# Optimization experiments

Hardware: AMD Instinct MI355X
Metric: run time of the kernel (lower is better)

Reference implementation:

```python
import jax, jax.numpy as jnp
import numpy as np

NUM_TREES = 150
ARITY = 4
DEPTH = 4
NUM_LEVELS = DEPTH + 1  # leaves (level 0) ... root (level DEPTH)
VOCAB = 10000
SUBTOK = 8
EMB_DIM = 256
HID = 256
NUM_CLASSES = 2


def _build_forest():
    # perfect ARITY-ary tree, level-order indexing; edges point child -> parent
    n = (ARITY ** (DEPTH + 1) - 1) // (ARITY - 1)  # 341
    src = np.arange(1, n)
    dst = (src - 1) // ARITY
    depth_of = np.zeros(n, dtype=np.int64)
    for j in range(1, n):
        depth_of[j] = depth_of[(j - 1) // ARITY] + 1
    level_of = DEPTH - depth_of  # leaves = 0, processed first (topo order)
    offs = np.arange(NUM_TREES) * n
    edge_src = (src[None, :] + offs[:, None]).ravel().astype(np.int32)
    edge_dst = (dst[None, :] + offs[:, None]).ravel().astype(np.int32)
    node_level = np.tile(level_of, NUM_TREES).astype(np.int32)
    graph_id = np.repeat(np.arange(NUM_TREES), n).astype(np.int32)
    leaf_mask = (node_level == 0).astype(np.int32)
    return edge_src, edge_dst, node_level, graph_id, leaf_mask, NUM_TREES * n


def setup_inputs() -> dict:
    key = jax.random.key(0)
    ks = jax.random.split(key, 16)
    es, ed, lvl, gid, lm, N = _build_forest()
    s_e = 1.0 / np.sqrt(EMB_DIM)
    s_h = 1.0 / np.sqrt(HID)
    s_f = 1.0 / np.sqrt(2 * HID)
    return {
        "node_feat1": jax.random.randint(ks[0], (N, SUBTOK), 0, VOCAB, dtype=jnp.int32),
        "node_feat2": jax.random.randint(ks[1], (N, SUBTOK), 0, VOCAB, dtype=jnp.int32),
        "emb1": jax.random.normal(ks[2], (VOCAB, EMB_DIM), jnp.float32) * 0.02,
        "emb2": jax.random.normal(ks[3], (VOCAB, EMB_DIM), jnp.float32) * 0.02,
        "W_iou1": jax.random.normal(ks[4], (EMB_DIM, 3 * HID), jnp.float32) * s_e,
        "W_iou2": jax.random.normal(ks[5], (EMB_DIM, 3 * HID), jnp.float32) * s_e,
        "U_iou1": jax.random.normal(ks[6], (HID, 3 * HID), jnp.float32) * s_h,
        "U_iou2": jax.random.normal(ks[7], (HID, 3 * HID), jnp.float32) * s_h,
        "Uf_W1": jax.random.normal(ks[8], (HID, HID), jnp.float32) * s_h,
        "Uf_b1": jnp.zeros((HID,), jnp.float32),
        "Uf_W2": jax.random.normal(ks[9], (HID, HID), jnp.float32) * s_h,
        "Uf_b2": jnp.zeros((HID,), jnp.float32),
        "b_iou1": jnp.zeros((3 * HID,), jnp.float32),
        "b_iou2": jnp.zeros((3 * HID,), jnp.float32),
        "Wf": jax.random.normal(ks[10], (2 * HID, NUM_CLASSES), jnp.float32) * s_f,
        "bf": jnp.zeros((NUM_CLASSES,), jnp.float32),
        "edge_src": jnp.asarray(es),
        "edge_dst": jnp.asarray(ed),
        "node_level": jnp.asarray(lvl),
        "graph_id": jnp.asarray(gid),
        "leaf_mask": jnp.asarray(lm),
    }


def _tree_lstm(iou0, U_iou, Uf_W, Uf_b, b_iou, edge_src, edge_dst, node_level):
    # ChildSum TreeLSTM, propagated level-by-level (leaves -> root)
    N = iou0.shape[0]
    h = jnp.zeros((N, HID), iou0.dtype)
    c = jnp.zeros((N, HID), iou0.dtype)
    for lvl in range(NUM_LEVELS):
        emask = (node_level[edge_dst] == lvl).astype(h.dtype)[:, None]  # [E,1]
        hs = h[edge_src] * emask  # children h (already computed at lower levels)
        f = jax.nn.sigmoid(hs @ Uf_W + Uf_b)  # per-edge forget gate
        h_tild = jax.ops.segment_sum(hs, edge_dst, num_segments=N)
        c_sum = jax.ops.segment_sum(f * c[edge_src] * emask, edge_dst, num_segments=N)
        has_child = jax.ops.segment_sum(emask, edge_dst, num_segments=N) > 0  # [N,1]
        # DGL semantics: reduce overwrites iou for internal nodes; leaves keep W_iou(x)*mask
        iou = jnp.where(has_child, h_tild @ U_iou, iou0) + b_iou
        i, o, u = jnp.split(iou, 3, axis=1)
        c_new = jax.nn.sigmoid(i) * jnp.tanh(u) + c_sum
        h_new = jax.nn.sigmoid(o) * jnp.tanh(c_new)
        at = (node_level == lvl)[:, None]
        h = jnp.where(at, h_new, h)
        c = jnp.where(at, c_new, c)
    return h


def _branch(node_feat, emb, W_iou, U_iou, Uf_W, Uf_b, b_iou,
            leaf_mask, edge_src, edge_dst, node_level, graph_id):
    embeds = emb[node_feat].mean(axis=1)  # subtoken mean pooling -> [N, EMB_DIM]
    iou0 = (embeds @ W_iou) * leaf_mask.astype(embeds.dtype)[:, None]
    h = _tree_lstm(iou0, U_iou, Uf_W, Uf_b, b_iou, edge_src, edge_dst, node_level)
    s = jax.ops.segment_sum(h, graph_id, num_segments=NUM_TREES)
    cnt = jax.ops.segment_sum(jnp.ones((h.shape[0],), h.dtype), graph_id, num_segments=NUM_TREES)
    return jax.nn.relu(s / cnt[:, None])  # mean graph readout + relu


def reference(node_feat1, node_feat2, emb1, emb2, W_iou1, W_iou2, U_iou1, U_iou2,
              Uf_W1, Uf_b1, Uf_W2, Uf_b2, b_iou1, b_iou2, Wf, bf,
              edge_src, edge_dst, node_level, graph_id, leaf_mask):
    m1 = _branch(node_feat1, emb1, W_iou1, U_iou1, Uf_W1, Uf_b1, b_iou1,
                 leaf_mask, edge_src, edge_dst, node_level, graph_id)
    m2 = _branch(node_feat2, emb2, W_iou2, U_iou2, Uf_W2, Uf_b2, b_iou2,
                 leaf_mask, edge_src, edge_dst, node_level, graph_id)
    logits = jax.nn.leaky_relu(jnp.concatenate([m1, m2], axis=1) @ Wf + bf, 0.01)
    return jax.nn.softmax(logits, axis=-1)
```

## Files before the change

kernel.cpp:

```cpp
#include <hip/hip_runtime.h>

#define NT 150
#define NPT 341
#define LEAF0 85
#define NL (NT*256)
#define NN (NT*NPT)
#define VOCAB 10000

typedef __attribute__((ext_vector_type(8))) short short8;
typedef __attribute__((ext_vector_type(4))) float floatx4;

__device__ __forceinline__ float sigf(float x){
  return __builtin_amdgcn_rcpf(1.0f + __expf(-x));
}
__device__ __forceinline__ float tanh_fast(float x){
  float e = __expf(2.0f*x);
  return 1.0f - 2.0f*__builtin_amdgcn_rcpf(e + 1.0f);
}
__device__ __forceinline__ float bf2f(ushort u){ union{unsigned i; float f;} v; v.i = ((unsigned)u)<<16; return v.f; }
__device__ __forceinline__ ushort f2bf(float x){ union{float f; unsigned i;} v; v.f = x; return (ushort)((v.i + 0x7fff + ((v.i>>16)&1))>>16); }

__global__ __launch_bounds__(256) void prep_k(
    const float* __restrict__ e1, const float* __restrict__ e2,
    ushort* __restrict__ E1, ushort* __restrict__ E2,
    const float* __restrict__ W1, const float* __restrict__ U1, const float* __restrict__ F1,
    const float* __restrict__ W2, const float* __restrict__ U2, const float* __restrict__ F2,
    ushort* Wt1, ushort* Ut1, ushort* Ft1, ushort* Wt2, ushort* Ut2, ushort* Ft2){
  __shared__ float T[32][33];
  int bid = blockIdx.x;
  if (bid < 5000){
    const float* s = (bid >= 2500) ? e2 : e1;
    ushort* d = (bid >= 2500) ? E2 : E1;
    size_t i = ((size_t)(bid % 2500)*256 + threadIdx.x)*4;
    float4 v = *(const float4*)&s[i];
    d[i+0]=f2bf(v.x); d[i+1]=f2bf(v.y); d[i+2]=f2bf(v.z); d[i+3]=f2bf(v.w);
    return;
  }
  int w = bid - 5000;
  int z = w / 192, rem = w % 192;
  int bx = rem % 24, by = rem / 24;
  const float* src; ushort* dst; int N;
  switch (z){
    case 0: src=W1; dst=Wt1; N=768; break;
    case 1: src=U1; dst=Ut1; N=768; break;
    case 2: src=F1; dst=Ft1; N=256; break;
    case 3: src=W2; dst=Wt2; N=768; break;
    case 4: src=U2; dst=Ut2; N=768; break;
    default: src=F2; dst=Ft2; N=256; break;
  }
  int n0 = bx*32; if (n0 >= N) return;
  int k0 = by*32;
  int nl = threadIdx.x & 31, kb = threadIdx.x >> 5;
  #pragma unroll
  for (int i=0;i<4;i++){ int kk = kb*4+i; T[kk][nl] = src[(size_t)(k0+kk)*N + n0 + nl]; }
  __syncthreads();
  #pragma unroll
  for (int i=0;i<4;i++){ int nn = kb*4+i; dst[(size_t)(n0+nn)*256 + k0 + nl] = f2bf(T[nl][nn]); }
}

__global__ __launch_bounds__(512) void leaf_gemm(
    const int* __restrict__ f1, const int* __restrict__ f2,
    const ushort* __restrict__ E1, const ushort* __restrict__ E2,
    const ushort* __restrict__ Wt1, const float* __restrict__ b1,
    const ushort* __restrict__ Wt2, const float* __restrict__ b2,
    ushort* __restrict__ h1, ushort* __restrict__ c1,
    ushort* __restrict__ h2, ushort* __restrict__ c2){
  __shared__ __attribute__((aligned(16))) ushort As[8][32*40];
  int br = blockIdx.y;
  const int* feat = br ? f2 : f1;
  const ushort* E = br ? E2 : E1;
  const ushort* Wt = br ? Wt2 : Wt1;
  const float* biou = br ? b2 : b1;
  ushort* h = br ? h2 : h1;
  ushort* c = br ? c2 : c1;
  int tid = threadIdx.x;
  int lane = tid & 63, wav = tid >> 6, quad = lane >> 4, l15 = lane & 15;
  int rowbase = blockIdx.x*32;

  {
    int row = tid >> 4, seg = tid & 15;
    int leaf = rowbase + row;
    int tree = leaf >> 8;
    size_t node = (size_t)tree*NPT + LEAF0 + (leaf & 255);
    const int* f = feat + node*8;
    int4 fA = *(const int4*)f;
    int4 fB = *(const int4*)(f+4);
    int idx[8] = {fA.x, fA.y, fA.z, fA.w, fB.x, fB.y, fB.z, fB.w};
    float s[16];
    #pragma unroll
    for (int q=0;q<16;q++) s[q]=0.f;
    #pragma unroll
    for (int half=0; half<2; half++){
      short8 va[4], vb[4];
      #pragma unroll
      for (int j=0;j<4;j++){
        const ushort* rowp = E + (size_t)idx[half*4+j]*256 + seg*16;
        va[j] = *(const short8*)rowp;
        vb[j] = *(const short8*)(rowp+8);
      }
      #pragma unroll
      for (int j=0;j<4;j++){
        #pragma unroll
        for (int q=0;q<8;q++){ s[q]+=bf2f((ushort)va[j][q]); s[8+q]+=bf2f((ushort)vb[j][q]); }
      }
    }
    short8 o1, o2;
    #pragma unroll
    for (int q=0;q<8;q++){ o1[q]=(short)f2bf(s[q]*0.125f); o2[q]=(short)f2bf(s[8+q]*0.125f); }
    int cch = seg >> 1, off = (seg & 1)*16;
    *(short8*)&As[cch][row*40 + off]     = o1;
    *(short8*)&As[cch][row*40 + off + 8] = o2;
  }
  __syncthreads();

  floatx4 acc[3][2][2];
  #pragma unroll
  for (int g=0;g<3;g++)
    #pragma unroll
    for (int cg=0;cg<2;cg++)
      #pragma unroll
      for (int r=0;r<2;r++) acc[g][cg][r] = (floatx4){0.f,0.f,0.f,0.f};

  const ushort* bp[3][2];
  #pragma unroll
  for (int g=0;g<3;g++)
    #pragma unroll
    for (int cg=0;cg<2;cg++)
      bp[g][cg] = Wt + (size_t)(g*256 + cg*128 + wav*16 + l15)*256 + quad*8;

  #pragma unroll
  for (int cch=0; cch<8; cch++){
    short8 B[3][2];
    #pragma unroll
    for (int g=0;g<3;g++)
      #pragma unroll
      for (int cg=0;cg<2;cg++) B[g][cg] = *(const short8*)(bp[g][cg] + cch*32);
    #pragma unroll
    for (int r=0;r<2;r++){
      short8 a = *(const short8*)&As[cch][(16*r + l15)*40 + quad*8];
      #pragma unroll
      for (int g=0;g<3;g++)
        #pragma unroll
        for (int cg=0;cg<2;cg++)
          acc[g][cg][r] = __builtin_amdgcn_mfma_f32_16x16x32_bf16(a, B[g][cg], acc[g][cg][r], 0,0,0);
    }
  }
  #pragma unroll
  for (int cg=0;cg<2;cg++){
    int hc = cg*128 + wav*16 + l15;
    float bi = biou[hc], bo = biou[256+hc], bu = biou[512+hc];
    #pragma unroll
    for (int r=0;r<2;r++){
      #pragma unroll
      for (int reg=0;reg<4;reg++){
        int leaf = rowbase + 16*r + quad*4 + reg;
        int tree = leaf >> 8;
        size_t node = (size_t)tree*NPT + LEAF0 + (leaf & 255);
        float iv = acc[0][cg][r][reg] + bi;
        float ov = acc[1][cg][r][reg] + bo;
        float uv = acc[2][cg][r][reg] + bu;
        float cc = sigf(iv)*tanh_fast(uv);
        float hh = sigf(ov)*tanh_fast(cc);
        h[node*256 + hc] = f2bf(hh);
        c[node*256 + hc] = f2bf(cc);
      }
    }
  }
}

__global__ __launch_bounds__(512) void level_k(
    const ushort* __restrict__ Ut1, const ushort* __restrict__ Ft1,
    const float* __restrict__ Ufb1, const float* __restrict__ bi1,
    const ushort* __restrict__ Ut2, const ushort* __restrict__ Ft2,
    const float* __restrict__ Ufb2, const float* __restrict__ bi2,
    ushort* __restrict__ h1, ushort* __restrict__ c1,
    ushort* __restrict__ h2, ushort* __restrict__ c2,
    int M, int shift, int base){
  __shared__ __attribute__((aligned(16))) ushort Ch[8][64*40];
  int br = blockIdx.z;
  const ushort* Ut = br ? Ut2 : Ut1;
  const ushort* Ft = br ? Ft2 : Ft1;
  const float* Ufb = br ? Ufb2 : Ufb1;
  const float* biou = br ? bi2 : bi1;
  ushort* h = br ? h2 : h1;
  ushort* c = br ? c2 : c1;
  int tid = threadIdx.x;
  int lane = tid & 63, wav = tid >> 6, quad = lane >> 4, l15 = lane & 15;
  int m0 = blockIdx.x*16;
  int mask = (1<<shift)-1;

  {
    int cl = tid >> 3, s8 = tid & 7;
    int sm = m0 + (cl >> 2); if (sm > M-1) sm = M-1;
    int stree = sm >> shift, sloc = base + (sm & mask);
    const ushort* sgp = h + ((size_t)stree*NPT + 4*sloc + 1 + (cl & 3))*256 + s8*32;
    short8 v0 = *(const short8*)(sgp);
    short8 v1 = *(const short8*)(sgp+8);
    short8 v2 = *(const short8*)(sgp+16);
    short8 v3 = *(const short8*)(sgp+24);
    *(short8*)&Ch[s8][cl*40 + 0]  = v0;
    *(short8*)&Ch[s8][cl*40 + 8]  = v1;
    *(short8*)&Ch[s8][cl*40 + 16] = v2;
    *(short8*)&Ch[s8][cl*40 + 24] = v3;
  }
  __syncthreads();

  int col = blockIdx.y*128 + wav*16 + l15;
  const ushort* bfp = Ft + (size_t)col*256 + quad*8;
  const ushort* bp0 = Ut + (size_t)(0*256 + col)*256 + quad*8;
  const ushort* bp1 = Ut + (size_t)(256 + col)*256 + quad*8;
  const ushort* bp2 = Ut + (size_t)(512 + col)*256 + quad*8;

  floatx4 af[4], ai[4], ao[4], au[4];
  #pragma unroll
  for (int r=0;r<4;r++){
    af[r] = (floatx4){0.f,0.f,0.f,0.f}; ai[r] = (floatx4){0.f,0.f,0.f,0.f};
    ao[r] = (floatx4){0.f,0.f,0.f,0.f}; au[r] = (floatx4){0.f,0.f,0.f,0.f};
  }

  #pragma unroll
  for (int cc=0; cc<8; cc++){
    short8 Bf = *(const short8*)(bfp + cc*32);
    short8 Bi = *(const short8*)(bp0 + cc*32);
    short8 Bo = *(const short8*)(bp1 + cc*32);
    short8 Bu = *(const short8*)(bp2 + cc*32);
    #pragma unroll
    for (int r=0;r<4;r++){
      short8 a = *(const short8*)&Ch[cc][(16*r + l15)*40 + quad*8];
      af[r] = __builtin_amdgcn_mfma_f32_16x16x32_bf16(a, Bf, af[r], 0,0,0);
      ai[r] = __builtin_amdgcn_mfma_f32_16x16x32_bf16(a, Bi, ai[r], 0,0,0);
      ao[r] = __builtin_amdgcn_mfma_f32_16x16x32_bf16(a, Bo, ao[r], 0,0,0);
      au[r] = __builtin_amdgcn_mfma_f32_16x16x32_bf16(a, Bu, au[r], 0,0,0);
    }
  }

  float ufb = Ufb[col];
  float bI = biou[col], bO = biou[256+col], bU = biou[512+col];
  #pragma unroll
  for (int r=0;r<4;r++){
    int m = m0 + 4*r + quad;
    int mm = m < M ? m : M-1;
    int tree = mm >> shift, loc = base + (mm & mask);
    size_t ch0 = ((size_t)tree*NPT + 4*loc + 1)*256 + col;
    float cs = 0.f;
    #pragma unroll
    for (int reg=0;reg<4;reg++)
      cs += sigf(af[r][reg] + ufb) * bf2f(c[ch0 + (size_t)reg*256]);
    float iv = ai[r][0]+ai[r][1]+ai[r][2]+ai[r][3] + bI;
    float ov = ao[r][0]+ao[r][1]+ao[r][2]+ao[r][3] + bO;
    float uv = au[r][0]+au[r][1]+au[r][2]+au[r][3] + bU;
    float cn = sigf(iv)*tanh_fast(uv) + cs;
    float hn = sigf(ov)*tanh_fast(cn);
    if (m < M){
      size_t off = ((size_t)tree*NPT + loc)*256 + col;
      h[off] = f2bf(hn);
      c[off] = f2bf(cn);
    }
  }
}

__global__ __launch_bounds__(256) void readout_k(
    const ushort* __restrict__ h1, const ushort* __restrict__ h2,
    float* __restrict__ mp1, float* __restrict__ mp2){
  __shared__ float red[4][256];
  int br = blockIdx.z, part = blockIdx.y, tree = blockIdx.x;
  const ushort* h = br ? h2 : h1;
  float* mp = br ? mp2 : mp1;
  int t = threadIdx.x;
  int lane = t & 63, rg = t >> 6;
  int start = part*85;
  int cnt = (part==3) ? 86 : 85;
  const ushort* base = h + ((size_t)tree*NPT + start)*256 + lane*4;
  float s0=0.f,s1=0.f,s2=0.f,s3=0.f;
  for (int i=rg; i<cnt; i+=4){
    ushort4 v = *(const ushort4*)(base + (size_t)i*256);
    s0 += bf2f(v.x); s1 += bf2f(v.y); s2 += bf2f(v.z); s3 += bf2f(v.w);
  }
  *(float4*)&red[rg][lane*4] = make_float4(s0,s1,s2,s3);
  __syncthreads();
  float tot = red[0][t]+red[1][t]+red[2][t]+red[3][t];
  mp[((size_t)tree*4 + part)*256 + t] = tot;
}

__global__ __launch_bounds__(64) void final_k(const float* __restrict__ mp1,
    const float* __restrict__ mp2, const float* __restrict__ Wf,
    const float* __restrict__ bf, float* __restrict__ out){
  int tree = blockIdx.x; int t = threadIdx.x;
  float p0=0.f, p1=0.f;
  for (int k=t;k<512;k+=64){
    const float* mp = (k<256) ? mp1 : mp2;
    int kk = k & 255;
    size_t b0 = ((size_t)tree*4)*256 + kk;
    float s = mp[b0] + mp[b0+256] + mp[b0+512] + mp[b0+768];
    float x = fmaxf(s*(1.0f/341.0f), 0.f);
    p0 += x*Wf[k*2+0]; p1 += x*Wf[k*2+1];
  }
  #pragma unroll
  for (int off=32; off>0; off>>=1){
    p0 += __shfl_down(p0, off);
    p1 += __shfl_down(p1, off);
  }
  if (t==0){
    float l0 = p0+bf[0], l1 = p1+bf[1];
    l0 = (l0>0.f)?l0:0.01f*l0;
    l1 = (l1>0.f)?l1:0.01f*l1;
    float mx = fmaxf(l0,l1);
    float e0 = __expf(l0-mx), e1 = __expf(l1-mx);
    float inv = 1.0f/(e0+e1);
    out[tree*2+0] = e0*inv; out[tree*2+1] = e1*inv;
  }
}

extern "C" void kernel_launch(void* const* d_in, const int* in_sizes, int n_in,
                              void* d_out, int out_size, void* d_ws, size_t ws_size,
                              hipStream_t stream) {
  const int*   feat1 = (const int*)  d_in[0];
  const int*   feat2 = (const int*)  d_in[1];
  const float* emb1  = (const float*)d_in[2];
  const float* emb2  = (const float*)d_in[3];
  const float* Wiou1 = (const float*)d_in[4];
  const float* Wiou2 = (const float*)d_in[5];
  const float* Uiou1 = (const float*)d_in[6];
  const float* Uiou2 = (const float*)d_in[7];
  const float* UfW1  = (const float*)d_in[8];
  const float* Ufb1  = (const float*)d_in[9];
  const float* UfW2  = (const float*)d_in[10];
  const float* Ufb2  = (const float*)d_in[11];
  const float* biou1 = (const float*)d_in[12];
  const float* biou2 = (const float*)d_in[13];
  const float* Wf    = (const float*)d_in[14];
  const float* bfv   = (const float*)d_in[15];
  float* out = (float*)d_out;

  char* ws = (char*)d_ws;
  ushort* h1  = (ushort*)ws;  ws += (size_t)NN*256*2;
  ushort* h2  = (ushort*)ws;  ws += (size_t)NN*256*2;
  ushort* c1  = (ushort*)ws;  ws += (size_t)NN*256*2;
  ushort* c2  = (ushort*)ws;  ws += (size_t)NN*256*2;
  ushort* E1  = (ushort*)ws;  ws += (size_t)VOCAB*256*2;
  ushort* E2  = (ushort*)ws;  ws += (size_t)VOCAB*256*2;
  ushort* Wt1 = (ushort*)ws;  ws += 768*256*2;
  ushort* Ut1 = (ushort*)ws;  ws += 768*256*2;
  ushort* Ft1 = (ushort*)ws;  ws += 256*256*2;
  ushort* Wt2 = (ushort*)ws;  ws += 768*256*2;
  ushort* Ut2 = (ushort*)ws;  ws += 768*256*2;
  ushort* Ft2 = (ushort*)ws;  ws += 256*256*2;
  float*  mp1 = (float*)ws;   ws += (size_t)NT*4*256*4;
  float*  mp2 = (float*)ws;   ws += (size_t)NT*4*256*4;

  prep_k<<<dim3(6152), 256, 0, stream>>>(emb1, emb2, E1, E2,
                                         Wiou1, Uiou1, UfW1, Wiou2, Uiou2, UfW2,
                                         Wt1, Ut1, Ft1, Wt2, Ut2, Ft2);
  leaf_gemm<<<dim3(NL/32, 2), 512, 0, stream>>>(feat1, feat2, E1, E2,
                                                Wt1, biou1, Wt2, biou2,
                                                h1, c1, h2, c2);

  const int lvlM[4]     = {9600, 2400, 600, 150};
  const int lvlShift[4] = {6, 4, 2, 0};
  const int lvlBase[4]  = {21, 5, 1, 0};
  for (int l=0;l<4;l++){
    int gx = (lvlM[l] + 15)/16;
    level_k<<<dim3(gx, 2, 2), 512, 0, stream>>>(Ut1, Ft1, Ufb1, biou1,
                                                Ut2, Ft2, Ufb2, biou2,
                                                h1, c1, h2, c2,
                                                lvlM[l], lvlShift[l], lvlBase[l]);
  }
  readout_k<<<dim3(NT, 4, 2), 256, 0, stream>>>(h1, h2, mp1, mp2);
  final_k<<<NT, 64, 0, stream>>>(mp1, mp2, Wf, bfv, out);
}
```

Before: 403.5 us.

## Fuse leaf GEMM with first tree level into one kernel

Merges the leaf embedding, W_iou GEMM and the first internal level update into a single kernel with 1024-thread blocks covering 64 leaves (16 parents). Leaf h values are kept in shared memory and c in registers, so the first level's U_iou and forget-gate GEMMs run without writing leaf state to global memory and reading it back. This drops one kernel launch and one level pass. The cost is heavier per-block register and LDS use and fewer blocks overall, which may reduce occupancy.

Measured after the change: 367.4 us. 1.1x faster.

```diff
diff --git a/kernel.cpp b/kernel.cpp
--- a/kernel.cpp
+++ b/kernel.cpp
@@ -58,30 +58,37 @@
   for (int i=0;i<4;i++){ int nn = kb*4+i; dst[(size_t)(n0+nn)*256 + k0 + nl] = f2bf(T[nl][nn]); }
 }
 
-__global__ __launch_bounds__(512) void leaf_gemm(
+__global__ __launch_bounds__(1024, 4) void leaf_lvl1_k(
     const int* __restrict__ f1, const int* __restrict__ f2,
     const ushort* __restrict__ E1, const ushort* __restrict__ E2,
-    const ushort* __restrict__ Wt1, const float* __restrict__ b1,
-    const ushort* __restrict__ Wt2, const float* __restrict__ b2,
+    const ushort* __restrict__ Wt1, const ushort* __restrict__ Ut1,
+    const ushort* __restrict__ Ft1, const float* __restrict__ b1,
+    const float* __restrict__ Ufb1,
+    const ushort* __restrict__ Wt2, const ushort* __restrict__ Ut2,
+    const ushort* __restrict__ Ft2, const float* __restrict__ b2,
+    const float* __restrict__ Ufb2,
     ushort* __restrict__ h1, ushort* __restrict__ c1,
     ushort* __restrict__ h2, ushort* __restrict__ c2){
-  __shared__ __attribute__((aligned(16))) ushort As[8][32*40];
+  __shared__ __attribute__((aligned(16))) ushort As[8][64*40];
   int br = blockIdx.y;
   const int* feat = br ? f2 : f1;
   const ushort* E = br ? E2 : E1;
   const ushort* Wt = br ? Wt2 : Wt1;
+  const ushort* Ut = br ? Ut2 : Ut1;
+  const ushort* Ft = br ? Ft2 : Ft1;
   const float* biou = br ? b2 : b1;
+  const float* Ufb = br ? Ufb2 : Ufb1;
   ushort* h = br ? h2 : h1;
   ushort* c = br ? c2 : c1;
   int tid = threadIdx.x;
   int lane = tid & 63, wav = tid >> 6, quad = lane >> 4, l15 = lane & 15;
-  int rowbase = blockIdx.x*32;
+  int rowbase = blockIdx.x*64;
+  int tree = rowbase >> 8, lbase = rowbase & 255;
+  size_t tb = (size_t)tree*NPT;
 
   {
     int row = tid >> 4, seg = tid & 15;
-    int leaf = rowbase + row;
-    int tree = leaf >> 8;
-    size_t node = (size_t)tree*NPT + LEAF0 + (leaf & 255);
+    size_t node = tb + LEAF0 + lbase + row;
     const int* f = feat + node*8;
     int4 fA = *(const int4*)f;
     int4 fB = *(const int4*)(f+4);
@@ -113,58 +120,97 @@
   }
   __syncthreads();
 
-  floatx4 acc[3][2][2];
+  floatx4 acc[3][4];
   #pragma unroll
   for (int g=0;g<3;g++)
     #pragma unroll
-    for (int cg=0;cg<2;cg++)
-      #pragma unroll
-      for (int r=0;r<2;r++) acc[g][cg][r] = (floatx4){0.f,0.f,0.f,0.f};
-
-  const ushort* bp[3][2];
-  #pragma unroll
-  for (int g=0;g<3;g++)
-    #pragma unroll
-    for (int cg=0;cg<2;cg++)
-      bp[g][cg] = Wt + (size_t)(g*256 + cg*128 + wav*16 + l15)*256 + quad*8;
+    for (int r=0;r<4;r++) acc[g][r] = (floatx4){0.f,0.f,0.f,0.f};
+
+  int hc = wav*16 + l15;
+  const ushort* bp0 = Wt + (size_t)(0*256 + hc)*256 + quad*8;
+  const ushort* bp1 = Wt + (size_t)(256 + hc)*256 + quad*8;
+  const ushort* bp2 = Wt + (size_t)(512 + hc)*256 + quad*8;
 
   #pragma unroll
   for (int cch=0; cch<8; cch++){
-    short8 B[3][2];
-    #pragma unroll
-    for (int g=0;g<3;g++)
-      #pragma unroll
-      for (int cg=0;cg<2;cg++) B[g][cg] = *(const short8*)(bp[g][cg] + cch*32);
-    #pragma unroll
-    for (int r=0;r<2;r++){
+    short8 b0 = *(const short8*)(bp0 + cch*32);
+    short8 b1 = *(const short8*)(bp1 + cch*32);
+    short8 b2 = *(const short8*)(bp2 + cch*32);
+    #pragma unroll
+    for (int r=0;r<4;r++){
       short8 a = *(const short8*)&As[cch][(16*r + l15)*40 + quad*8];
-      #pragma unroll
-      for (int g=0;g<3;g++)
-        #pragma unroll
-        for (int cg=0;cg<2;cg++)
-          acc[g][cg][r] = __builtin_amdgcn_mfma_f32_16x16x32_bf16(a, B[g][cg], acc[g][cg][r], 0,0,0);
-    }
-  }
-  #pragma unroll
-  for (int cg=0;cg<2;cg++){
-    int hc = cg*128 + wav*16 + l15;
-    float bi = biou[hc], bo = biou[256+hc], bu = biou[512+hc];
-    #pragma unroll
-    for (int r=0;r<2;r++){
-      #pragma unroll
-      for (int reg=0;reg<4;reg++){
-        int leaf = rowbase + 16*r + quad*4 + reg;
-        int tree = leaf >> 8;
-        size_t node = (size_t)tree*NPT + LEAF0 + (leaf & 255);
-        float iv = acc[0][cg][r][reg] + bi;
-        float ov = acc[1][cg][r][reg] + bo;
-        float uv = acc[2][cg][r][reg] + bu;
-        float cc = sigf(iv)*tanh_fast(uv);
-        float hh = sigf(ov)*tanh_fast(cc);
-        h[node*256 + hc] = f2bf(hh);
-        c[node*256 + hc] = f2bf(cc);
-      }
-    }
+      acc[0][r] = __builtin_amdgcn_mfma_f32_16x16x32_bf16(a, b0, acc[0][r], 0,0,0);
+      acc[1][r] = __builtin_amdgcn_mfma_f32_16x16x32_bf16(a, b1, acc[1][r], 0,0,0);
+      acc[2][r] = __builtin_amdgcn_mfma_f32_16x16x32_bf16(a, b2, acc[2][r], 0,0,0);
+    }
+  }
+  __syncthreads();
+
+  float bi = biou[hc], bo = biou[256+hc], bu = biou[512+hc];
+  float cv[16];
+  #pragma unroll
+  for (int r=0;r<4;r++){
+    #pragma unroll
+    for (int reg=0;reg<4;reg++){
+      int row = 16*r + quad*4 + reg;
+      float iv = acc[0][r][reg] + bi;
+      float ov = acc[1][r][reg] + bo;
+      float uv = acc[2][r][reg] + bu;
+      float cc = sigf(iv)*tanh_fast(uv);
+      float hh = sigf(ov)*tanh_fast(cc);
+      cv[4*r+reg] = cc;
+      ushort hb = f2bf(hh);
+      h[(tb + LEAF0 + lbase + row)*256 + hc] = hb;
+      As[hc>>5][row*40 + (hc & 31)] = hb;
+    }
+  }
+  __syncthreads();
+
+  const ushort* bfp = Ft + (size_t)hc*256 + quad*8;
+  const ushort* up0 = Ut + (size_t)(0*256 + hc)*256 + quad*8;
+  const ushort* up1 = Ut + (size_t)(256 + hc)*256 + quad*8;
+  const ushort* up2 = Ut + (size_t)(512 + hc)*256 + quad*8;
+
+  floatx4 af[4], ai[4], ao[4], au[4];
+  #pragma unroll
+  for (int r=0;r<4;r++){
+    af[r] = (floatx4){0.f,0.f,0.f,0.f}; ai[r] = (floatx4){0.f,0.f,0.f,0.f};
+    ao[r] = (floatx4){0.f,0.f,0.f,0.f}; au[r] = (floatx4){0.f,0.f,0.f,0.f};
+  }
+  #pragma unroll
+  for (int cch=0; cch<8; cch++){
+    short8 Bf = *(const short8*)(bfp + cch*32);
+    short8 Bi = *(const short8*)(up0 + cch*32);
+    short8 Bo = *(const short8*)(up1 + cch*32);
+    short8 Bu = *(const short8*)(up2 + cch*32);
+    #pragma unroll
+    for (int r=0;r<4;r++){
+      short8 a = *(const short8*)&As[cch][(16*r + l15)*40 + quad*8];
+      af[r] = __builtin_amdgcn_mfma_f32_16x16x32_bf16(a, Bf, af[r], 0,0,0);
+      ai[r] = __builtin_amdgcn_mfma_f32_16x16x32_bf16(a, Bi, ai[r], 0,0,0);
+      ao[r] = __builtin_amdgcn_mfma_f32_16x16x32_bf16(a, Bo, ao[r], 0,0,0);
+      au[r] = __builtin_amdgcn_mfma_f32_16x16x32_bf16(a, Bu, au[r], 0,0,0);
+    }
+  }
+
+  int nodebase = 21 + (lbase >> 2);
+  float ufb = Ufb[hc];
+  float bI = biou[hc], bO = biou[256+hc], bU = biou[512+hc];
+  #pragma unroll
+  for (int r=0;r<4;r++){
+    int m_local = 4*r + quad;
+    float cs = 0.f;
+    #pragma unroll
+    for (int reg=0;reg<4;reg++)
+      cs += sigf(af[r][reg] + ufb) * cv[4*r+reg];
+    float iv = ai[r][0]+ai[r][1]+ai[r][2]+ai[r][3] + bI;
+    float ov = ao[r][0]+ao[r][1]+ao[r][2]+ao[r][3] + bO;
+    float uv = au[r][0]+au[r][1]+au[r][2]+au[r][3] + bU;
+    float cn = sigf(iv)*tanh_fast(uv) + cs;
+    float hn = sigf(ov)*tanh_fast(cn);
+    size_t off = (tb + nodebase + m_local)*256 + hc;
+    h[off] = f2bf(hn);
+    c[off] = f2bf(cn);
   }
 }
 
@@ -351,14 +397,15 @@
   prep_k<<<dim3(6152), 256, 0, stream>>>(emb1, emb2, E1, E2,
                                          Wiou1, Uiou1, UfW1, Wiou2, Uiou2, UfW2,
                                          Wt1, Ut1, Ft1, Wt2, Ut2, Ft2);
-  leaf_gemm<<<dim3(NL/32, 2), 512, 0, stream>>>(feat1, feat2, E1, E2,
-                                                Wt1, biou1, Wt2, biou2,
-                                                h1, c1, h2, c2);
-
-  const int lvlM[4]     = {9600, 2400, 600, 150};
-  const int lvlShift[4] = {6, 4, 2, 0};
-  const int lvlBase[4]  = {21, 5, 1, 0};
-  for (int l=0;l<4;l++){
+  leaf_lvl1_k<<<dim3(NL/64, 2), 1024, 0, stream>>>(feat1, feat2, E1, E2,
+                                                   Wt1, Ut1, Ft1, biou1, Ufb1,
+                                                   Wt2, Ut2, Ft2, biou2, Ufb2,
+                                                   h1, c1, h2, c2);
+
+  const int lvlM[3]     = {2400, 600, 150};
+  const int lvlShift[3] = {4, 2, 0};
+  const int lvlBase[3]  = {5, 1, 0};
+  for (int l=0;l<3;l++){
     int gx = (lvlM[l] + 15)/16;
     level_k<<<dim3(gx, 2, 2), 512, 0, stream>>>(Ut1, Ft1, Ufb1, biou1,
                                                 Ut2, Ft2, Ufb2, biou2,
```
